# Performance work log

Measured on AMD Instinct MI355X. Metric: run time of the kernel, lower is better.

The kernel has to match this reference:

```python
import jax, jax.numpy as jnp
import numpy as np

B, Q, D_MODEL, H, D_HEAD, PAGE, N_PAGES = 8, 1024, 2048, 16, 128, 256, 8


def setup_inputs() -> dict:
    key = jax.random.key(0)
    ks = jax.random.split(key, 6)
    hidden_states = jax.random.normal(ks[0], (B, Q, D_MODEL), jnp.float32) * 0.02
    W_attn = jax.random.normal(ks[1], (D_MODEL, 3 * D_MODEL), jnp.float32) * 0.02
    b_attn = jnp.zeros((3 * D_MODEL,), jnp.float32)
    W_proj = jax.random.normal(ks[2], (D_MODEL, D_MODEL), jnp.float32) * 0.02
    b_proj = jnp.zeros((D_MODEL,), jnp.float32)
    k_pages = jax.random.normal(ks[3], (N_PAGES, B, H, PAGE, D_HEAD), jnp.float32)
    v_pages = jax.random.normal(ks[4], (N_PAGES, B, H, PAGE, D_HEAD), jnp.float32)
    # every cached page fully valid: (start=0, length=PAGE)
    page_pos = jnp.broadcast_to(jnp.array([0, PAGE], jnp.int32), (N_PAGES, B, 2))
    # current chunk: starts at end of cache, length = q_len
    input_pos = jnp.broadcast_to(jnp.array([N_PAGES * PAGE, Q], jnp.int32), (B, 2))
    return {
        "hidden_states": hidden_states,
        "W_attn": W_attn, "b_attn": b_attn,
        "W_proj": W_proj, "b_proj": b_proj,
        "k_pages": k_pages, "v_pages": v_pages,
        "page_pos": page_pos, "input_pos": input_pos,
    }


def reference(hidden_states, W_attn, b_attn, W_proj, b_proj,
              k_pages, v_pages, page_pos, input_pos):
    dtype = hidden_states.dtype
    NEG = jnp.finfo(dtype).min
    b, q_len, d_model = hidden_states.shape
    n_pages, _, num_heads, page_size, d_head = k_pages.shape
    scale = 1.0 / d_head ** 0.5

    # qkv projection (GPT2 c_attn)
    qkv = hidden_states @ W_attn + b_attn
    q, k_curr, v_curr = jnp.split(qkv, 3, axis=-1)

    def split_heads(x):  # [b, q, d_model] -> [b, h, q, d_head]
        return x.reshape(b, q_len, num_heads, d_head).transpose(0, 2, 1, 3)

    q = split_heads(q)
    k_curr = split_heads(k_curr)
    v_curr = split_heads(v_curr)

    # online softmax state
    m0 = jnp.full((b, num_heads, q_len, 1), NEG, dtype)
    l0 = jnp.zeros((b, num_heads, q_len, 1), dtype)
    acc0 = jnp.zeros((b, num_heads, q_len, d_head), dtype)

    kv_idx = jnp.arange(page_size)

    def page_step(carry, page):
        m, l, acc = carry
        k_p, v_p, pos = page  # [b,h,p,d], [b,h,p,d], [b,2]
        start, length = pos[:, 0], pos[:, 1]
        valid = (kv_idx[None, :] >= start[:, None]) & \
                (kv_idx[None, :] < (start + length)[:, None])  # [b, p]
        s = jnp.einsum('bhqd,bhpd->bhqp', q, k_p) * scale
        s = jnp.where(valid[:, None, None, :], s, NEG)
        m_p = s.max(axis=-1, keepdims=True)
        m_new = jnp.maximum(m, m_p)
        alpha = jnp.exp(m - m_new)
        e = jnp.exp(s - m_new)
        acc = alpha * acc + jnp.einsum('bhqp,bhpd->bhqd', e, v_p)
        l = alpha * l + e.sum(axis=-1, keepdims=True)
        return (m_new, l, acc), None

    (m, l, acc), _ = jax.lax.scan(page_step, (m0, l0, acc0),
                                  (k_pages, v_pages, page_pos))

    # final pass over current chunk: aligned start = 0, length from input_pos
    length = input_pos[:, 1]
    q_idx = jnp.arange(q_len)
    valid = q_idx[None, :] < length[:, None]                     # [b, q]
    causal = jnp.tril(jnp.ones((q_len, q_len), bool))            # keep lower tri
    s = jnp.einsum('bhqd,bhkd->bhqk', q, k_curr) * scale
    keep = valid[:, None, None, :] & causal[None, None, :, :]
    s = jnp.where(keep, s, NEG)
    m_p = s.max(axis=-1, keepdims=True)
    m_new = jnp.maximum(m, m_p)
    alpha = jnp.exp(m - m_new)
    e = jnp.exp(s - m_new)
    acc = alpha * acc + jnp.einsum('bhqk,bhkd->bhqd', e, v_curr)
    l = alpha * l + e.sum(axis=-1, keepdims=True)

    context = acc / jnp.maximum(l, 1e-9)
    context = context.transpose(0, 2, 1, 3).reshape(b, q_len, d_model)
    out = context @ W_proj + b_proj  # resid_dropout is identity in eval
    return out
```

## Files before the change

kernel.cpp:

```cpp
#include <hip/hip_runtime.h>

typedef __bf16 bf16;
typedef __bf16 bf16x8 __attribute__((ext_vector_type(8)));
typedef __bf16 bf16x4 __attribute__((ext_vector_type(4)));
typedef float f32x4 __attribute__((ext_vector_type(4)));
typedef unsigned short u16x4 __attribute__((ext_vector_type(4)));
typedef __attribute__((address_space(3))) const void as3_void;
typedef __attribute__((address_space(3))) const char as3_char;

#define GLOAD16(G,L) __builtin_amdgcn_global_load_lds((__attribute__((address_space(1))) const void*)(G), (__attribute__((address_space(3))) void*)(L), 16, 0, 0)

__global__ void k_cvt_bf16(const float* __restrict__ src, bf16* __restrict__ dst, int n4){
  int i = blockIdx.x*256 + threadIdx.x;
  if (i < n4){
    float4 v = reinterpret_cast<const float4*>(src)[i];
    bf16x4 o; o[0]=(bf16)v.x; o[1]=(bf16)v.y; o[2]=(bf16)v.z; o[3]=(bf16)v.w;
    reinterpret_cast<bf16x4*>(dst)[i] = o;
  }
}

__global__ void k_transpose_cvt(const float* __restrict__ src, bf16* __restrict__ dst, int K, int N){
  __shared__ float tile[32][33];
  int n0 = blockIdx.x*32, k0 = blockIdx.y*32;
  int tx = threadIdx.x & 31, ty = threadIdx.x >> 5;
  #pragma unroll
  for (int i=0;i<32;i+=8)
    tile[ty+i][tx] = src[(size_t)(k0+ty+i)*N + n0+tx];
  __syncthreads();
  #pragma unroll
  for (int i=0;i<32;i+=8)
    dst[(size_t)(n0+ty+i)*K + k0+tx] = (bf16)tile[tx][ty+i];
}

template<int EPI>
__global__ __launch_bounds__(512,2) void k_gemm8(
    const bf16* __restrict__ A, const bf16* __restrict__ Bt,
    const float* __restrict__ bias, int N, int K,
    bf16* __restrict__ q_out, bf16* __restrict__ k_out, bf16* __restrict__ v_out,
    float* __restrict__ c_out)
{
  __shared__ bf16 S[2][4][8192];
  const int t = threadIdx.x, w = t>>6, l = t&63, g = l>>4, c = l&15;
  const int wm = w>>2, wn = w&3;
  const int nb = N>>8;
  const int cpx = gridDim.x>>3;
  const int swz = (blockIdx.x&7)*cpx + (blockIdx.x>>3);
  const int m0 = (swz/nb)<<8, n0 = (swz%nb)<<8;
  const int NK = K>>6;

  int abase[2];
  #pragma unroll
  for (int kk=0; kk<2; ++kk)
    abase[kk] = (c<<7) + (((((kk<<2)|g)) ^ (c&7))<<4);

  const int r0 = t>>3;
  const int col0 = ((t&7) ^ (r0&7))<<3;

  auto stageA = [&](int kt2){
    #pragma unroll
    for (int hh=0; hh<2; ++hh){
      const bf16* sp = A + (size_t)(m0 + hh*128)*K + (kt2<<6);
      char* dp = (char*)&S[kt2&1][hh][0];
      GLOAD16(sp + (size_t)r0*K + col0,      dp + t*16);
      GLOAD16(sp + (size_t)(r0+64)*K + col0, dp + (t+512)*16);
    }
  };
  auto stageB = [&](int kt2){
    #pragma unroll
    for (int hh=0; hh<2; ++hh){
      const bf16* sp = Bt + (size_t)(n0 + hh*128)*K + (kt2<<6);
      char* dp = (char*)&S[kt2&1][2+hh][0];
      GLOAD16(sp + (size_t)r0*K + col0,      dp + t*16);
      GLOAD16(sp + (size_t)(r0+64)*K + col0, dp + (t+512)*16);
    }
  };

  f32x4 acc[8][4] = {};

  stageA(0); stageB(0);
  asm volatile("s_waitcnt vmcnt(0)" ::: "memory");
  __builtin_amdgcn_s_barrier();

  for (int kt=0; kt<NK; ++kt){
    const int bufc = kt&1;
    const char* Ab_ = (const char*)&S[bufc][wm][0];
    const char* Bb_ = (const char*)&S[bufc][2+(wn>>1)][0] + ((wn&1)<<13);
    const bool pre = (kt+1 < NK);
    bf16x8 af[4][2], bfr[2][2];

    auto lda = [&](int mh){
      #pragma unroll
      for (int mf=0; mf<4; ++mf)
        #pragma unroll
        for (int kk=0; kk<2; ++kk)
          af[mf][kk] = *reinterpret_cast<const bf16x8*>(Ab_ + abase[kk] + mh*8192 + mf*2048);
    };
    auto ldb = [&](int nh){
      #pragma unroll
      for (int nf=0; nf<2; ++nf)
        #pragma unroll
        for (int kk=0; kk<2; ++kk)
          bfr[nf][kk] = *reinterpret_cast<const bf16x8*>(Bb_ + abase[kk] + nh*4096 + nf*2048);
    };
    auto cluster = [&](int mh, int nh){
      __builtin_amdgcn_s_barrier();
      asm volatile("s_waitcnt lgkmcnt(0)" ::: "memory");
      __builtin_amdgcn_sched_barrier(0);
      __builtin_amdgcn_s_setprio(1);
      #pragma unroll
      for (int mf=0; mf<4; ++mf)
        #pragma unroll
        for (int nf=0; nf<2; ++nf)
          #pragma unroll
          for (int kk=0; kk<2; ++kk)
            acc[mh*4+mf][nh*2+nf] =
              __builtin_amdgcn_mfma_f32_16x16x32_bf16(af[mf][kk], bfr[nf][kk], acc[mh*4+mf][nh*2+nf], 0,0,0);
      __builtin_amdgcn_s_setprio(0);
    };

    lda(0); ldb(0);
    if (pre) stageA(kt+1);
    cluster(0,0);
    __builtin_amdgcn_s_barrier();
    ldb(1);
    if (pre) stageB(kt+1);
    cluster(0,1);
    __builtin_amdgcn_s_barrier();
    lda(1);
    cluster(1,1);
    __builtin_amdgcn_s_barrier();
    ldb(0);
    cluster(1,0);
    asm volatile("s_waitcnt vmcnt(0)" ::: "memory");
    __builtin_amdgcn_s_barrier();
  }

  if constexpr (EPI==0){
    #pragma unroll
    for (int NF=0; NF<4; ++NF){
      const int col = n0 + wn*64 + NF*16 + c;
      const int sec = col>>11; const int rem = col&2047;
      const int hhd = rem>>7;  const int dd = rem&127;
      bf16* dst = (sec==0) ? q_out : ((sec==1) ? k_out : v_out);
      const float bv = bias[col];
      const float qs = (sec==0) ? 0.12751743f : 1.0f;
      #pragma unroll
      for (int MF=0; MF<8; ++MF)
        #pragma unroll
        for (int ri=0; ri<4; ++ri){
          const int row = m0 + wm*128 + MF*16 + (g<<2) + ri;
          const int bb = row>>10, qp = row&1023;
          dst[(((size_t)(bb*16+hhd)*1024 + qp)<<7) + dd] = (bf16)((acc[MF][NF][ri] + bv)*qs);
        }
    }
  } else {
    #pragma unroll
    for (int NF=0; NF<4; ++NF){
      const int col = n0 + wn*64 + NF*16 + c;
      const float bv = bias[col];
      #pragma unroll
      for (int MF=0; MF<8; ++MF)
        #pragma unroll
        for (int ri=0; ri<4; ++ri){
          const int row = m0 + wm*128 + MF*16 + (g<<2) + ri;
          c_out[(size_t)row*N + col] = acc[MF][NF][ri] + bv;
        }
    }
  }
}

#define TRRD(R0, R1, O0, O1) \
  asm volatile("ds_read_b64_tr_b16 %0, %2 offset:" O0 "\n\t" \
               "ds_read_b64_tr_b16 %1, %2 offset:" O1 \
               : "=&v"(R0), "=&v"(R1) : "v"(vbL) : "memory")

__global__ __launch_bounds__(512) __attribute__((amdgpu_waves_per_eu(4,4))) void k_attn(
    const bf16* __restrict__ qb, const bf16* __restrict__ kb, const bf16* __restrict__ vb,
    const bf16* __restrict__ kpb, const bf16* __restrict__ vpb,
    const int* __restrict__ page_pos, const int* __restrict__ input_pos,
    bf16* __restrict__ ctx)
{
  __shared__ bf16 Ks[2*64*128];
  __shared__ bf16 Vs[2*64*128];
  const int t = threadIdx.x, w = t>>6, l = t&63, g = l>>4, c = l&15;
  const int bid = blockIdx.x;
  const int wg = (bid&7)*128 + (bid>>3);
  const int qt = wg & 7, h = (wg>>3)&15, b = wg>>7;
  const int q0w = (qt<<7) + (w<<4);
  const size_t bh = (size_t)(b*16 + h);

  const bf16* qptr = qb + (bh<<17);
  bf16x8 qf[4];
  #pragma unroll
  for (int kc=0;kc<4;kc++)
    qf[kc] = *reinterpret_cast<const bf16x8*>(qptr + ((size_t)(q0w + c)<<7) + kc*32 + (g<<3));

  int kbase[4];
  #pragma unroll
  for (int kc=0;kc<4;kc++)
    kbase[kc] = (c<<8) + ((((kc<<2)|g) ^ c)<<4);
  const int voffL = (g<<11) + (c<<3);

  int kOff[2], vOff[2];
  #pragma unroll
  for (int j=0;j<2;j++){
    const int slot = t + (j<<9);
    {
      const int a = slot<<4; const int r = a>>8; const int co = (a&255) ^ ((r&15)<<4);
      kOff[j] = (r<<7) + (co>>1);
    }
    {
      const int s_ = slot;
      const int p  = ((s_>>6)<<2) | ((s_>>1)&3);
      const int d0 = (((s_>>3)&7)<<4) | ((s_&1)<<3);
      const int pp = (p&32) | ((p&4)<<2) | (((p>>3)&3)<<2) | (p&3);
      vOff[j] = (pp<<7) + d0;
    }
  }
  const bf16* kcb = kb + (bh<<17);
  const bf16* vcb = vb + (bh<<17);
  const int len_b = input_pos[b*2+1];
  const int NT = 32 + ((qt+1)<<1);

  f32x4 o[8] = {};
  float mrow = -1e38f;
  float lsum = 0.f;

  auto tsrc = [&](int T, const bf16*& ks, const bf16*& vs_){
    if (T < 32){
      size_t pb = ((((size_t)(T>>2)<<3) + (size_t)b)*16 + (size_t)h) << 15;
      size_t off = (size_t)(T&3)<<13;
      ks = kpb + pb + off; vs_ = vpb + pb + off;
    } else {
      int kt = T-32; ks = kcb + ((size_t)kt<<13); vs_ = vcb + ((size_t)kt<<13);
    }
  };
  auto stage = [&](int T, int buf){
    const bf16 *ks, *vs_; tsrc(T, ks, vs_);
    char* kd = (char*)Ks + (buf<<14) + (w<<10);
    char* vd = (char*)Vs + (buf<<14) + (w<<10);
    #pragma unroll
    for (int j=0;j<2;j++){
      GLOAD16(ks  + kOff[j], kd + (j<<13));
      GLOAD16(vs_ + vOff[j], vd + (j<<13));
    }
  };

  auto process = [&](int buf, int lo, int hi, bool masked, bool causal, int ktg){
    const char* Kb = (const char*)Ks + (buf<<14);
    as3_char* vbL = (as3_char*)((as3_char*)Vs + (buf<<14) + voffL);
    f32x4 s[4] = {};
    #pragma unroll
    for (int kc=0;kc<4;kc++){
      const char* bk = Kb + kbase[kc];
      bf16x8 kf[4];
      #pragma unroll
      for (int cb=0;cb<4;cb++)
        kf[cb] = *reinterpret_cast<const bf16x8*>(bk + (cb<<12));
      __builtin_amdgcn_s_setprio(1);
      #pragma unroll
      for (int cb=0;cb<4;cb++)
        s[cb] = __builtin_amdgcn_mfma_f32_16x16x32_bf16(kf[cb], qf[kc], s[cb], 0,0,0);
      __builtin_amdgcn_s_setprio(0);
    }
    if (masked){
      #pragma unroll
      for (int cb=0;cb<4;cb++)
        #pragma unroll
        for (int ri=0;ri<4;ri++){
          const int kvl = (cb<<4) + (g<<2) + ri;
          bool ok = (kvl >= lo) && (kvl < hi);
          if (causal) ok = ok && ((ktg + kvl) <= (q0w + c));
          s[cb][ri] = ok ? s[cb][ri] : -3e38f;
        }
    }
    {
      float m0_ = fmaxf(fmaxf(s[0][0], s[0][1]), fmaxf(s[0][2], s[0][3]));
      float m1_ = fmaxf(fmaxf(s[1][0], s[1][1]), fmaxf(s[1][2], s[1][3]));
      float m2_ = fmaxf(fmaxf(s[2][0], s[2][1]), fmaxf(s[2][2], s[2][3]));
      float m3_ = fmaxf(fmaxf(s[3][0], s[3][1]), fmaxf(s[3][2], s[3][3]));
      float mx = fmaxf(fmaxf(m0_, m1_), fmaxf(m2_, m3_));
      const int defer = __all(mx - mrow <= 11.5f);
      if (!defer){
        float mr = fmaxf(mx, __shfl_xor(mx, 16, 64));
        mr = fmaxf(mr, __shfl_xor(mr, 32, 64));
        const float mn = fmaxf(mrow, mr);
        const float al = exp2f(mrow - mn);
        mrow = mn;
        lsum *= al;
        #pragma unroll
        for (int ri=0;ri<4;ri++){
          const float av = __shfl(al, (l&48) | ((g<<2)+ri), 64);
          #pragma unroll
          for (int dcb=0;dcb<8;dcb++) o[dcb][ri] *= av;
        }
      }
      float ps = 0.f;
      #pragma unroll
      for (int cb=0;cb<4;cb++)
        #pragma unroll
        for (int ri=0;ri<4;ri++){
          const float e = exp2f(s[cb][ri] - mrow);
          s[cb][ri] = e; ps += e;
        }
      lsum += ps;
    }
    {
      u16x4 vr0[4], vr1[4];
      bf16x8 pav;
      union { unsigned short us[8]; bf16x8 v; } uu;
      #pragma unroll
      for (int e=0;e<8;e++) pav[e] = (bf16)s[e>>2][e&3];
      TRRD(vr0[0],vr1[0],"0","1024");  TRRD(vr0[1],vr1[1],"128","1152");
      TRRD(vr0[2],vr1[2],"256","1280");TRRD(vr0[3],vr1[3],"384","1408");
      asm volatile("s_waitcnt lgkmcnt(0)" ::: "memory");
      __builtin_amdgcn_sched_barrier(0);
      __builtin_amdgcn_s_setprio(1);
      #pragma unroll
      for (int d4=0;d4<4;d4++){
        #pragma unroll
        for (int i=0;i<4;i++){ uu.us[i]=vr0[d4][i]; uu.us[4+i]=vr1[d4][i]; }
        o[d4] = __builtin_amdgcn_mfma_f32_16x16x32_bf16(pav, uu.v, o[d4], 0,0,0);
      }
      __builtin_amdgcn_s_setprio(0);
      TRRD(vr0[0],vr1[0],"512","1536");  TRRD(vr0[1],vr1[1],"640","1664");
      TRRD(vr0[2],vr1[2],"768","1792");  TRRD(vr0[3],vr1[3],"896","1920");
      asm volatile("s_waitcnt lgkmcnt(0)" ::: "memory");
      __builtin_amdgcn_sched_barrier(0);
      __builtin_amdgcn_s_setprio(1);
      #pragma unroll
      for (int d4=0;d4<4;d4++){
        #pragma unroll
        for (int i=0;i<4;i++){ uu.us[i]=vr0[d4][i]; uu.us[4+i]=vr1[d4][i]; }
        o[4+d4] = __builtin_amdgcn_mfma_f32_16x16x32_bf16(pav, uu.v, o[4+d4], 0,0,0);
      }
      __builtin_amdgcn_s_setprio(0);
      #pragma unroll
      for (int e=0;e<8;e++) pav[e] = (bf16)s[2+(e>>2)][e&3];
      TRRD(vr0[0],vr1[0],"8192","9216"); TRRD(vr0[1],vr1[1],"8320","9344");
      TRRD(vr0[2],vr1[2],"8448","9472"); TRRD(vr0[3],vr1[3],"8576","9600");
      asm volatile("s_waitcnt lgkmcnt(0)" ::: "memory");
      __builtin_amdgcn_sched_barrier(0);
      __builtin_amdgcn_s_setprio(1);
      #pragma unroll
      for (int d4=0;d4<4;d4++){
        #pragma unroll
        for (int i=0;i<4;i++){ uu.us[i]=vr0[d4][i]; uu.us[4+i]=vr1[d4][i]; }
        o[d4] = __builtin_amdgcn_mfma_f32_16x16x32_bf16(pav, uu.v, o[d4], 0,0,0);
      }
      __builtin_amdgcn_s_setprio(0);
      TRRD(vr0[0],vr1[0],"8704","9728"); TRRD(vr0[1],vr1[1],"8832","9856");
      TRRD(vr0[2],vr1[2],"8960","9984"); TRRD(vr0[3],vr1[3],"9088","10112");
      asm volatile("s_waitcnt lgkmcnt(0)" ::: "memory");
      __builtin_amdgcn_sched_barrier(0);
      __builtin_amdgcn_s_setprio(1);
      #pragma unroll
      for (int d4=0;d4<4;d4++){
        #pragma unroll
        for (int i=0;i<4;i++){ uu.us[i]=vr0[d4][i]; uu.us[4+i]=vr1[d4][i]; }
        o[4+d4] = __builtin_amdgcn_mfma_f32_16x16x32_bf16(pav, uu.v, o[4+d4], 0,0,0);
      }
      __builtin_amdgcn_s_setprio(0);
    }
  };

  int buf = 0;
  stage(0, 0);
  asm volatile("s_waitcnt vmcnt(0)" ::: "memory");
  __syncthreads();
  for (int T=0; T<NT; ++T){
    if (T+1 < NT) stage(T+1, buf^1);
    int lo=0, hi=64, ktg=0; bool causal=false, masked=false, skip=false;
    if (T < 32){
      const int pg = T>>2, to = T&3;
      const int start = page_pos[(pg*8+b)*2], plen = page_pos[(pg*8+b)*2+1];
      lo = start - (to<<6); hi = start + plen - (to<<6); if (hi>64) hi=64;
      masked = (lo > 0) || (hi < 64);
      skip = (hi <= 0) || (lo >= 64);
    } else {
      const int kt = T-32; ktg = kt<<6;
      hi = len_b - ktg; if (hi>64) hi=64;
      skip = (ktg > q0w + 15) || (hi <= 0);
      causal = (ktg + 63 > q0w);
      masked = causal || (hi < 64);
    }
    if (!skip) process(buf, lo, hi, masked, causal, ktg);
    asm volatile("s_waitcnt vmcnt(0)" ::: "memory");
    __syncthreads();
    buf ^= 1;
  }

  {
    float tl = lsum;
    tl += __shfl_xor(tl, 16, 64);
    tl += __shfl_xor(tl, 32, 64);
    const float inv = 1.f / fmaxf(tl, 1e-9f);
    #pragma unroll
    for (int ri=0;ri<4;ri++){
      const float iv = __shfl(inv, (l&48) | ((g<<2)+ri), 64);
      const int q = q0w + (g<<2) + ri;
      #pragma unroll
      for (int dcb=0;dcb<8;dcb++)
        ctx[(((size_t)(b<<10) + q)<<11) + (h<<7) + (dcb<<4) + c] = (bf16)(o[dcb][ri]*iv);
    }
  }
}

extern "C" void kernel_launch(void* const* d_in, const int* in_sizes, int n_in,
                              void* d_out, int out_size, void* d_ws, size_t ws_size,
                              hipStream_t stream)
{
  const float* hidden  = (const float*)d_in[0];
  const float* W_attn  = (const float*)d_in[1];
  const float* b_attn  = (const float*)d_in[2];
  const float* W_proj  = (const float*)d_in[3];
  const float* b_proj  = (const float*)d_in[4];
  const float* k_pages = (const float*)d_in[5];
  const float* v_pages = (const float*)d_in[6];
  const int*   page_pos  = (const int*)d_in[7];
  const int*   input_pos = (const int*)d_in[8];
  float* out = (float*)d_out;
  char* ws = (char*)d_ws;
  bf16* A1  = (bf16*)(ws);
  bf16* Wt1 = (bf16*)(ws + 33554432);
  bf16* Wt2 = (bf16*)(ws + 58720256);
  bf16* qb  = (bf16*)(ws + 67108864);
  bf16* kb  = (bf16*)(ws + 100663296);
  bf16* vb  = (bf16*)(ws + 134217728);
  bf16* kpb = (bf16*)(ws + 167772160);
  bf16* vpb = (bf16*)(ws + 234881024);
  bf16* ctx = A1;

  k_cvt_bf16<<<16384, 256, 0, stream>>>(hidden, A1, 4194304);
  k_cvt_bf16<<<32768, 256, 0, stream>>>(k_pages, kpb, 8388608);
  k_cvt_bf16<<<32768, 256, 0, stream>>>(v_pages, vpb, 8388608);
  k_transpose_cvt<<<dim3(192,64), 256, 0, stream>>>(W_attn, Wt1, 2048, 6144);
  k_transpose_cvt<<<dim3(64,64),  256, 0, stream>>>(W_proj, Wt2, 2048, 2048);
  k_gemm8<0><<<768, 512, 0, stream>>>(A1, Wt1, b_attn, 6144, 2048, qb, kb, vb, nullptr);
  k_attn<<<1024, 512, 0, stream>>>(qb, kb, vb, kpb, vpb, page_pos, input_pos, ctx);
  k_gemm8<1><<<256, 512, 0, stream>>>(ctx, Wt2, b_proj, 2048, 2048, nullptr, nullptr, nullptr, out);
}
```

Before: 648.8 us.

## Fuse fp32-to-bf16 conversion of KV pages into attention tile staging

Removes the two standalone conversion kernels for k_pages and v_pages. The attention kernel now reads the fp32 pages directly, converts them in registers and writes bf16 into the swizzled LDS layout. The paged-tile loads are issued after the current tile's compute, not before it as async global-to-LDS copies. This saves a full fp32 read plus bf16 write and reread of 512 MB of cache data, but doubles the bytes read per tile inside attention and weakens load/compute overlap for the paged portion.

After: 631.0 us. -2.7%, faster.

```diff
diff --git a/kernel.cpp b/kernel.cpp
--- a/kernel.cpp
+++ b/kernel.cpp
@@ -176,7 +176,7 @@
 
 __global__ __launch_bounds__(512) __attribute__((amdgpu_waves_per_eu(4,4))) void k_attn(
     const bf16* __restrict__ qb, const bf16* __restrict__ kb, const bf16* __restrict__ vb,
-    const bf16* __restrict__ kpb, const bf16* __restrict__ vpb,
+    const float* __restrict__ kpf, const float* __restrict__ vpf,
     const int* __restrict__ page_pos, const int* __restrict__ input_pos,
     bf16* __restrict__ ctx)
 {
@@ -217,6 +217,22 @@
       vOff[j] = (pp<<7) + d0;
     }
   }
+  int ksrc[4], vsrc[4];
+  #pragma unroll
+  for (int j=0;j<4;j++){
+    const int uu = t + (j<<9);
+    const int s_ = uu>>1, hh = uu&1;
+    {
+      const int a = s_<<4; const int r = a>>8; const int co = (a&255) ^ ((r&15)<<4);
+      ksrc[j] = (r<<7) + (co>>1) + (hh<<2);
+    }
+    {
+      const int p  = ((s_>>6)<<2) | ((s_>>1)&3);
+      const int d0 = (((s_>>3)&7)<<4) | ((s_&1)<<3);
+      const int pp = (p&32) | ((p&4)<<2) | (((p>>3)&3)<<2) | (p&3);
+      vsrc[j] = (pp<<7) + d0 + (hh<<2);
+    }
+  }
   const bf16* kcb = kb + (bh<<17);
   const bf16* vcb = vb + (bh<<17);
   const int len_b = input_pos[b*2+1];
@@ -226,23 +242,39 @@
   float mrow = -1e38f;
   float lsum = 0.f;
 
-  auto tsrc = [&](int T, const bf16*& ks, const bf16*& vs_){
-    if (T < 32){
-      size_t pb = ((((size_t)(T>>2)<<3) + (size_t)b)*16 + (size_t)h) << 15;
-      size_t off = (size_t)(T&3)<<13;
-      ks = kpb + pb + off; vs_ = vpb + pb + off;
-    } else {
-      int kt = T-32; ks = kcb + ((size_t)kt<<13); vs_ = vcb + ((size_t)kt<<13);
-    }
-  };
-  auto stage = [&](int T, int buf){
-    const bf16 *ks, *vs_; tsrc(T, ks, vs_);
+  auto stage_causal = [&](int T, int buf){
+    const int kt = T-32;
+    const bf16* ks  = kcb + ((size_t)kt<<13);
+    const bf16* vs_ = vcb + ((size_t)kt<<13);
     char* kd = (char*)Ks + (buf<<14) + (w<<10);
     char* vd = (char*)Vs + (buf<<14) + (w<<10);
     #pragma unroll
     for (int j=0;j<2;j++){
       GLOAD16(ks  + kOff[j], kd + (j<<13));
       GLOAD16(vs_ + vOff[j], vd + (j<<13));
+    }
+  };
+  auto stage_paged = [&](int T, int buf){
+    const size_t pb  = ((((size_t)(T>>2)<<3) + (size_t)b)*16 + (size_t)h) << 15;
+    const size_t off = (size_t)(T&3)<<13;
+    const float* kp = kpf + pb + off;
+    const float* vp = vpf + pb + off;
+    float4 kr[4], vr_[4];
+    #pragma unroll
+    for (int j=0;j<4;j++) kr[j]  = *reinterpret_cast<const float4*>(kp + ksrc[j]);
+    #pragma unroll
+    for (int j=0;j<4;j++) vr_[j] = *reinterpret_cast<const float4*>(vp + vsrc[j]);
+    char* kd = (char*)Ks + (buf<<14);
+    char* vd = (char*)Vs + (buf<<14);
+    #pragma unroll
+    for (int j=0;j<4;j++){
+      bf16x4 o4; o4[0]=(bf16)kr[j].x; o4[1]=(bf16)kr[j].y; o4[2]=(bf16)kr[j].z; o4[3]=(bf16)kr[j].w;
+      *reinterpret_cast<bf16x4*>(kd + ((t + (j<<9))<<3)) = o4;
+    }
+    #pragma unroll
+    for (int j=0;j<4;j++){
+      bf16x4 o4; o4[0]=(bf16)vr_[j].x; o4[1]=(bf16)vr_[j].y; o4[2]=(bf16)vr_[j].z; o4[3]=(bf16)vr_[j].w;
+      *reinterpret_cast<bf16x4*>(vd + ((t + (j<<9))<<3)) = o4;
     }
   };
 
@@ -365,11 +397,12 @@
   };
 
   int buf = 0;
-  stage(0, 0);
-  asm volatile("s_waitcnt vmcnt(0)" ::: "memory");
+  stage_paged(0, 0);
   __syncthreads();
   for (int T=0; T<NT; ++T){
-    if (T+1 < NT) stage(T+1, buf^1);
+    const bool pre = (T+1 < NT);
+    const bool np  = pre && (T+1 < 32);
+    if (pre && !np) stage_causal(T+1, buf^1);
     int lo=0, hi=64, ktg=0; bool causal=false, masked=false, skip=false;
     if (T < 32){
       const int pg = T>>2, to = T&3;
@@ -385,6 +418,7 @@
       masked = causal || (hi < 64);
     }
     if (!skip) process(buf, lo, hi, masked, causal, ktg);
+    if (np) stage_paged(T+1, buf^1);
     asm volatile("s_waitcnt vmcnt(0)" ::: "memory");
     __syncthreads();
     buf ^= 1;
@@ -427,16 +461,12 @@
   bf16* qb  = (bf16*)(ws + 67108864);
   bf16* kb  = (bf16*)(ws + 100663296);
   bf16* vb  = (bf16*)(ws + 134217728);
-  bf16* kpb = (bf16*)(ws + 167772160);
-  bf16* vpb = (bf16*)(ws + 234881024);
   bf16* ctx = A1;
 
   k_cvt_bf16<<<16384, 256, 0, stream>>>(hidden, A1, 4194304);
-  k_cvt_bf16<<<32768, 256, 0, stream>>>(k_pages, kpb, 8388608);
-  k_cvt_bf16<<<32768, 256, 0, stream>>>(v_pages, vpb, 8388608);
   k_transpose_cvt<<<dim3(192,64), 256, 0, stream>>>(W_attn, Wt1, 2048, 6144);
   k_transpose_cvt<<<dim3(64,64),  256, 0, stream>>>(W_proj, Wt2, 2048, 2048);
   k_gemm8<0><<<768, 512, 0, stream>>>(A1, Wt1, b_attn, 6144, 2048, qb, kb, vb, nullptr);
-  k_attn<<<1024, 512, 0, stream>>>(qb, kb, vb, kpb, vpb, page_pos, input_pos, ctx);
+  k_attn<<<1024, 512, 0, stream>>>(qb, kb, vb, k_pages, v_pages, page_pos, input_pos, ctx);
   k_gemm8<1><<<256, 512, 0, stream>>>(ctx, Wt2, b_proj, 2048, 2048, nullptr, nullptr, nullptr, out);
 }
```

## Fuse KV page bf16 conversion into QKV GEMM launch as extra blocks

Applied to the files above, without the earlier changes.

Removes the two separate fp32-to-bf16 conversion launches for the K/V page caches. Instead, 256 extra blocks are appended to the QKV GEMM grid and grid-stride convert the pages. The memory-bound conversion is meant to overlap with the compute-bound GEMM and cut launch overhead. The risk is that conversion blocks occupy CU slots and memory bandwidth, delaying GEMM tiles.

After: 712.3 us. 1.1x slower.

```diff
diff --git a/kernel.cpp b/kernel.cpp
--- a/kernel.cpp
+++ b/kernel.cpp
@@ -37,7 +37,9 @@
     const bf16* __restrict__ A, const bf16* __restrict__ Bt,
     const float* __restrict__ bias, int N, int K,
     bf16* __restrict__ q_out, bf16* __restrict__ k_out, bf16* __restrict__ v_out,
-    float* __restrict__ c_out)
+    float* __restrict__ c_out,
+    const float* __restrict__ kpf, const float* __restrict__ vpf,
+    bf16* __restrict__ kpb, bf16* __restrict__ vpb, int nTiles)
 {
   __shared__ bf16 S[2][4][8192];
   const int t = threadIdx.x, w = t>>6, l = t&63, g = l>>4, c = l&15;
@@ -45,6 +47,25 @@
   const int nb = N>>8;
   const int cpx = gridDim.x>>3;
   const int swz = (blockIdx.x&7)*cpx + (blockIdx.x>>3);
+  if (swz >= nTiles){
+    const int ci = swz - nTiles;
+    const int stride = (gridDim.x - nTiles)*512;
+    const float4* ks = (const float4*)kpf;
+    const float4* vs = (const float4*)vpf;
+    bf16x4* kd = (bf16x4*)kpb;
+    bf16x4* vd = (bf16x4*)vpb;
+    for (int i = ci*512 + t; i < 8388608; i += stride){
+      float4 v = ks[i];
+      bf16x4 o4; o4[0]=(bf16)v.x; o4[1]=(bf16)v.y; o4[2]=(bf16)v.z; o4[3]=(bf16)v.w;
+      kd[i] = o4;
+    }
+    for (int i = ci*512 + t; i < 8388608; i += stride){
+      float4 v = vs[i];
+      bf16x4 o4; o4[0]=(bf16)v.x; o4[1]=(bf16)v.y; o4[2]=(bf16)v.z; o4[3]=(bf16)v.w;
+      vd[i] = o4;
+    }
+    return;
+  }
   const int m0 = (swz/nb)<<8, n0 = (swz%nb)<<8;
   const int NK = K>>6;
 
@@ -432,11 +453,11 @@
   bf16* ctx = A1;
 
   k_cvt_bf16<<<16384, 256, 0, stream>>>(hidden, A1, 4194304);
-  k_cvt_bf16<<<32768, 256, 0, stream>>>(k_pages, kpb, 8388608);
-  k_cvt_bf16<<<32768, 256, 0, stream>>>(v_pages, vpb, 8388608);
   k_transpose_cvt<<<dim3(192,64), 256, 0, stream>>>(W_attn, Wt1, 2048, 6144);
   k_transpose_cvt<<<dim3(64,64),  256, 0, stream>>>(W_proj, Wt2, 2048, 2048);
-  k_gemm8<0><<<768, 512, 0, stream>>>(A1, Wt1, b_attn, 6144, 2048, qb, kb, vb, nullptr);
+  k_gemm8<0><<<1024, 512, 0, stream>>>(A1, Wt1, b_attn, 6144, 2048, qb, kb, vb, nullptr,
+                                       k_pages, v_pages, kpb, vpb, 768);
   k_attn<<<1024, 512, 0, stream>>>(qb, kb, vb, kpb, vpb, page_pos, input_pos, ctx);
-  k_gemm8<1><<<256, 512, 0, stream>>>(ctx, Wt2, b_proj, 2048, 2048, nullptr, nullptr, nullptr, out);
+  k_gemm8<1><<<256, 512, 0, stream>>>(ctx, Wt2, b_proj, 2048, 2048, nullptr, nullptr, nullptr, out,
+                                      nullptr, nullptr, nullptr, nullptr, 256);
 }
```
